# Kernel tuning notes

Measured on AMD Instinct MI355X. Metric: run time of the kernel, lower is better.

Reference implementation:

```python
import jax, jax.numpy as jnp
import numpy as np

N_NODES = 100000
N_EDGES = 1600000
IN_CH = 128
OUT_CH = 64
HID = 2 * OUT_CH  # 128


def setup_inputs() -> dict:
    key = jax.random.key(0)
    ks = jax.random.split(key, 8)
    s = lambda fan_in: 1.0 / np.sqrt(fan_in)
    return {
        "x": jax.random.normal(ks[0], (N_NODES, IN_CH), jnp.float32),
        "edge_index": jax.random.randint(ks[1], (2, N_EDGES), 0, N_NODES, dtype=jnp.int32),
        "W1": jax.random.normal(ks[2], (IN_CH, HID), jnp.float32) * s(IN_CH),
        "b1": jnp.zeros((HID,), jnp.float32),
        "W2": jax.random.normal(ks[3], (HID, HID), jnp.float32) * s(HID),
        "b2": jnp.zeros((HID,), jnp.float32),
        "W3": jax.random.normal(ks[4], (HID, OUT_CH), jnp.float32) * s(HID),
        "b3": jnp.zeros((OUT_CH,), jnp.float32),
    }


def reference(x, edge_index, W1, b1, W2, b2, W3, b3):
    N = x.shape[0]
    # GCNConv (PyG semantics): add self-loops, symmetric deg^{-1/2} normalization,
    # linear transform, scatter-add aggregation at destination, then bias.
    loops = jnp.arange(N, dtype=edge_index.dtype)
    src = jnp.concatenate([edge_index[0], loops])  # [E+N]
    dst = jnp.concatenate([edge_index[1], loops])  # [E+N]
    deg = jnp.zeros((N,), x.dtype).at[dst].add(1.0)  # in-degree incl. self-loop
    dinv = jnp.where(deg > 0, jax.lax.rsqrt(deg), 0.0)
    norm = (dinv[src] * dinv[dst])[:, None]  # [E+N, 1]

    def gcn_conv(h, W, b):
        h = h @ W  # transform first (smaller when out < in)
        msg = h[src] * norm  # gather + normalize, [E+N, C]
        agg = jnp.zeros((N, h.shape[1]), h.dtype).at[dst].add(msg)  # scatter-add
        return agg + b

    h = jax.nn.relu(gcn_conv(x, W1, b1))
    h = jax.nn.relu(gcn_conv(h, W2, b2))
    h = gcn_conv(h, W3, b3)
    return jnp.min(h, axis=0)  # min-pool over nodes -> [OUT_CH]
```

## Files before the change

### kernel.cpp

```cpp
#include <hip/hip_runtime.h>
#include <stdint.h>
#include <stddef.h>
#include <float.h>

typedef short bf16x8 __attribute__((ext_vector_type(8)));
typedef float f32x4 __attribute__((ext_vector_type(4)));

static __device__ __forceinline__ unsigned enc_min(float v) {
  unsigned u = __float_as_uint(v);
  return (u & 0x80000000u) ? ~u : (u | 0x80000000u);
}
static __device__ __forceinline__ unsigned short f2bf(float f) {
  unsigned u = __float_as_uint(f);
  u += 0x7fffu + ((u >> 16) & 1u);
  return (unsigned short)(u >> 16);
}
static __device__ __forceinline__ float bf2f(unsigned short b) {
  return __uint_as_float(((unsigned)b) << 16);
}
static __device__ __forceinline__ void acc8(float* a, uint4 v) {
  a[0] += __uint_as_float(v.x << 16);
  a[1] += __uint_as_float(v.x & 0xffff0000u);
  a[2] += __uint_as_float(v.y << 16);
  a[3] += __uint_as_float(v.y & 0xffff0000u);
  a[4] += __uint_as_float(v.z << 16);
  a[5] += __uint_as_float(v.z & 0xffff0000u);
  a[6] += __uint_as_float(v.w << 16);
  a[7] += __uint_as_float(v.w & 0xffff0000u);
}

__global__ __launch_bounds__(256) void k_count_bin(const int* __restrict__ edge, int E, int N,
                                                   int* __restrict__ cnt8,
                                                   int* __restrict__ bin_cur,
                                                   int2* __restrict__ pairs,
                                                   int binw, int bcap) {
  __shared__ int h[8], gbase[8], lfill[8];
  int cslot = blockIdx.x & 7;
  int* cnt = cnt8 + (size_t)cslot * N;
  int tid = threadIdx.x;
  int nt = (E + 1023) >> 10;
  for (int t = blockIdx.x; t < nt; t += gridDim.x) {
    int e0 = t << 10;
    if (tid < 8) { h[tid] = 0; lfill[tid] = 0; }
    __syncthreads();
    int d[4], s[4], g[4], r[4];
#pragma unroll
    for (int k = 0; k < 4; ++k) {
      int e = e0 + tid + k * 256;
      d[k] = -1;
      if (e < E) {
        d[k] = edge[E + e];
        s[k] = edge[e];
        g[k] = (int)((unsigned)d[k] / (unsigned)binw);
        r[k] = atomicAdd(&cnt[d[k]], 1);
        atomicAdd(&h[g[k]], 1);
      }
    }
    __syncthreads();
    if (tid < 8) gbase[tid] = atomicAdd(&bin_cur[tid], h[tid]);
    __syncthreads();
#pragma unroll
    for (int k = 0; k < 4; ++k) {
      if (d[k] >= 0) {
        int rr = atomicAdd(&lfill[g[k]], 1);
        int p = gbase[g[k]] + rr;
        unsigned packed = (unsigned)d[k] | ((unsigned)cslot << 17) | ((unsigned)r[k] << 20);
        if (p < bcap) pairs[(size_t)g[k] * bcap + p] = make_int2((int)packed, s[k]);
      }
    }
    __syncthreads();
  }
}

__global__ void k_scan1(const int* __restrict__ cnt8, int N,
                        int* __restrict__ cnt, int* __restrict__ incl,
                        int* __restrict__ bsum) {
  __shared__ int sm[1024];
  int tid = threadIdx.x;
  int i = blockIdx.x * 1024 + tid;
  int v = 0;
  if (i < N) {
#pragma unroll
    for (int g = 0; g < 8; ++g) v += cnt8[(size_t)g * N + i];
    cnt[i] = v;
  }
  sm[tid] = v;
  __syncthreads();
  for (int off = 1; off < 1024; off <<= 1) {
    int t = (tid >= off) ? sm[tid - off] : 0;
    __syncthreads();
    sm[tid] += t;
    __syncthreads();
  }
  if (i < N) incl[i] = sm[tid];
  if (tid == 1023) bsum[blockIdx.x] = sm[1023];
}

__global__ void k_scan2(const int* __restrict__ bsum, int nb, int* __restrict__ boff) {
  __shared__ int sm[128];
  int tid = threadIdx.x;
  int v = (tid < nb) ? bsum[tid] : 0;
  sm[tid] = v;
  __syncthreads();
  for (int off = 1; off < 128; off <<= 1) {
    int t = (tid >= off) ? sm[tid - off] : 0;
    __syncthreads();
    sm[tid] += t;
    __syncthreads();
  }
  if (tid < nb) boff[tid] = sm[tid] - v;
}

__global__ void k_aux(const int* __restrict__ cnt, const int* __restrict__ cnt8,
                      const int* __restrict__ incl, const int* __restrict__ boff,
                      int N, int E, int* __restrict__ row_ptr,
                      int* __restrict__ base8, float* __restrict__ dinv) {
  int i = blockIdx.x * blockDim.x + threadIdx.x;
  if (i < N) {
    int rp = incl[i] - cnt[i] + boff[i >> 10];
    row_ptr[i] = rp;
    dinv[i] = 1.0f / sqrtf((float)(cnt[i] + 1));
    int run = rp;
#pragma unroll
    for (int c = 0; c < 8; ++c) {
      base8[(size_t)c * N + i] = run;
      run += cnt8[(size_t)c * N + i];
    }
  } else if (i == N) {
    row_ptr[N] = E;
  }
}

__global__ void k_prepw(const float* __restrict__ W1, const float* __restrict__ W2,
                        const float* __restrict__ W3,
                        unsigned short* __restrict__ w1h, unsigned short* __restrict__ w1l,
                        unsigned short* __restrict__ w2h, unsigned short* __restrict__ w2l,
                        unsigned short* __restrict__ w3h, unsigned short* __restrict__ w3l) {
  const int K = 128;
  int idx = blockIdx.x * 256 + threadIdx.x;
  const float* W;
  unsigned short *oh, *ol;
  int Nn, base;
  if (idx < 16384) { W = W1; Nn = 128; oh = w1h; ol = w1l; base = idx; }
  else if (idx < 32768) { W = W2; Nn = 128; oh = w2h; ol = w2l; base = idx - 16384; }
  else if (idx < 40960) { W = W3; Nn = 64; oh = w3h; ol = w3l; base = idx - 32768; }
  else return;
  int n = base / K, k = base % K;
  float w = W[(size_t)k * Nn + n];
  unsigned short h = f2bf(w);
  unsigned short l = f2bf(w - bf2f(h));
  int nf = n >> 4, mloc = n & 15, kci = k >> 5, quad = (k >> 3) & 3, j = k & 7;
  size_t o = ((size_t)((nf * 4 + kci) * 64 + quad * 16 + mloc)) * 8 + j;
  oh[o] = h;
  ol[o] = l;
}

template <int NFW>
static __device__ __forceinline__ void gemm_body(const float* __restrict__ A,
                                                 const unsigned short* __restrict__ Wfh,
                                                 const unsigned short* __restrict__ Wfl,
                                                 const float* __restrict__ dinv,
                                                 unsigned short* __restrict__ P, int M,
                                                 int blk) {
  const int K = 128;
  const int COUT = NFW * 64;
  __shared__ unsigned short Ah[64][136];
  __shared__ unsigned short Al[64][136];
  int tid = threadIdx.x;
  int m0 = blk * 64;
  int w = tid >> 6, lane = tid & 63;

  bf16x8 bh[NFW][4], bl[NFW][4];
#pragma unroll
  for (int i = 0; i < NFW; ++i)
#pragma unroll
    for (int kci = 0; kci < 4; ++kci) {
      size_t o = ((size_t)(((w * NFW + i) * 4 + kci) * 64 + lane)) * 8;
      bh[i][kci] = *(const bf16x8*)&Wfh[o];
      bl[i][kci] = *(const bf16x8*)&Wfl[o];
    }

#pragma unroll
  for (int q = 0; q < 8; ++q) {
    int f = q * 256 + tid;
    int m = f >> 5, k4 = f & 31;
    int row = m0 + m;
    if (row >= M) row = M - 1;
    float4 v = *(const float4*)&A[(size_t)row * K + k4 * 4];
    unsigned short h0 = f2bf(v.x), h1 = f2bf(v.y), h2 = f2bf(v.z), h3 = f2bf(v.w);
    unsigned short l0 = f2bf(v.x - bf2f(h0)), l1 = f2bf(v.y - bf2f(h1));
    unsigned short l2 = f2bf(v.z - bf2f(h2)), l3 = f2bf(v.w - bf2f(h3));
    uint2 hh, ll;
    hh.x = (unsigned)h0 | ((unsigned)h1 << 16);
    hh.y = (unsigned)h2 | ((unsigned)h3 << 16);
    ll.x = (unsigned)l0 | ((unsigned)l1 << 16);
    ll.y = (unsigned)l2 | ((unsigned)l3 << 16);
    *(uint2*)&Ah[m][k4 * 4] = hh;
    *(uint2*)&Al[m][k4 * 4] = ll;
  }
  __syncthreads();

  int mloc = lane & 15, quad = lane >> 4;
  f32x4 acc[4][NFW];
#pragma unroll
  for (int rt = 0; rt < 4; ++rt)
#pragma unroll
    for (int i = 0; i < NFW; ++i) acc[rt][i] = (f32x4){0.f, 0.f, 0.f, 0.f};

#pragma unroll
  for (int rt = 0; rt < 4; ++rt) {
    const unsigned short* ph = &Ah[rt * 16 + mloc][quad * 8];
    const unsigned short* pl = &Al[rt * 16 + mloc][quad * 8];
#pragma unroll
    for (int kci = 0; kci < 4; ++kci) {
      bf16x8 ah = *(const bf16x8*)(ph + kci * 32);
      bf16x8 al = *(const bf16x8*)(pl + kci * 32);
#pragma unroll
      for (int i = 0; i < NFW; ++i) {
        acc[rt][i] = __builtin_amdgcn_mfma_f32_16x16x32_bf16(al, bh[i][kci], acc[rt][i], 0, 0, 0);
        acc[rt][i] = __builtin_amdgcn_mfma_f32_16x16x32_bf16(ah, bl[i][kci], acc[rt][i], 0, 0, 0);
        acc[rt][i] = __builtin_amdgcn_mfma_f32_16x16x32_bf16(ah, bh[i][kci], acc[rt][i], 0, 0, 0);
      }
    }
  }

#pragma unroll
  for (int rt = 0; rt < 4; ++rt) {
    int rbase = m0 + rt * 16 + quad * 4;
#pragma unroll
    for (int r = 0; r < 4; ++r) {
      int row = rbase + r;
      if (row < M) {
        float dv = dinv[row];
#pragma unroll
        for (int i = 0; i < NFW; ++i) {
          int nf = w * NFW + i;
          P[(size_t)row * COUT + nf * 16 + mloc] = f2bf(acc[rt][i][r] * dv);
        }
      }
    }
  }
}

__global__ __launch_bounds__(256) void k_fill_gemm(const float* __restrict__ A,
                                                   const unsigned short* __restrict__ Wfh,
                                                   const unsigned short* __restrict__ Wfl,
                                                   const float* __restrict__ dinv,
                                                   unsigned short* __restrict__ P, int M,
                                                   const int2* __restrict__ pairs,
                                                   const int* __restrict__ bin_cur, int bcap,
                                                   const int* __restrict__ base8, int N,
                                                   int* __restrict__ srcs, int ns) {
  if ((int)blockIdx.x >= ns) {
    gemm_body<2>(A, Wfh, Wfl, dinv, P, M, blockIdx.x - ns);
  } else {
    int grp = blockIdx.x & 7;
    int bslot = blockIdx.x >> 3;
    int nslot = ns >> 3;
    int cnt_g = bin_cur[grp];
    if (cnt_g > bcap) cnt_g = bcap;
    const int2* pp = pairs + (size_t)grp * bcap;
    for (int i = bslot * blockDim.x + threadIdx.x; i < cnt_g; i += nslot * blockDim.x) {
      int2 pr = pp[i];
      unsigned w = (unsigned)pr.x;
      int d = (int)(w & 0x1FFFFu);
      int c = (int)((w >> 17) & 7u);
      int r = (int)(w >> 20);
      srcs[base8[(size_t)c * N + d] + r] = pr.y;
    }
  }
}

template <int NFW>
__global__ __launch_bounds__(256) void k_agg_gemm(const unsigned short* __restrict__ Pin,
                                                  const int* __restrict__ row_ptr,
                                                  const int* __restrict__ srcs,
                                                  const float* __restrict__ dinv,
                                                  const float* __restrict__ bias,
                                                  const unsigned short* __restrict__ Wfh,
                                                  const unsigned short* __restrict__ Wfl,
                                                  unsigned short* __restrict__ Pout, int N) {
  const int COUT = NFW * 64;
  __shared__ unsigned short Ah[16][136];
  __shared__ unsigned short Al[16][136];
  int tid = threadIdx.x;
  int wv = tid >> 6, lane = tid & 63;
  int grp = lane >> 4, sub = lane & 15;
  int m = wv * 4 + grp;
  int d = blockIdx.x * 16 + m;
  int dc = d < N ? d : N - 1;
  bool valid = d < N;
  unsigned soff = (unsigned)sub * 16u;
  const char* Pb = (const char*)Pin;

  float a[8] = {0.f, 0.f, 0.f, 0.f, 0.f, 0.f, 0.f, 0.f};
  {
    uint4 v = *(const uint4*)(Pb + ((unsigned)dc * 256u + soff));
    acc8(a, v);
  }
  int lo = row_ptr[dc];
  int hi = row_ptr[valid ? d + 1 : dc];
  int j = lo;
  for (; j + 8 <= hi; j += 8) {
    unsigned id[8];
    uint4 vv[8];
#pragma unroll
    for (int k = 0; k < 8; ++k) id[k] = (unsigned)srcs[j + k];
#pragma unroll
    for (int k = 0; k < 8; ++k) vv[k] = *(const uint4*)(Pb + (id[k] * 256u + soff));
#pragma unroll
    for (int k = 0; k < 8; ++k) acc8(a, vv[k]);
  }
  for (; j + 4 <= hi; j += 4) {
    unsigned id[4];
    uint4 vv[4];
#pragma unroll
    for (int k = 0; k < 4; ++k) id[k] = (unsigned)srcs[j + k];
#pragma unroll
    for (int k = 0; k < 4; ++k) vv[k] = *(const uint4*)(Pb + (id[k] * 256u + soff));
#pragma unroll
    for (int k = 0; k < 4; ++k) acc8(a, vv[k]);
  }
  for (; j < hi; ++j) {
    unsigned i0 = (unsigned)srcs[j];
    uint4 v0 = *(const uint4*)(Pb + (i0 * 256u + soff));
    acc8(a, v0);
  }

  bf16x8 bh[NFW][4], bl[NFW][4];
#pragma unroll
  for (int i = 0; i < NFW; ++i)
#pragma unroll
    for (int kci = 0; kci < 4; ++kci) {
      size_t o = ((size_t)(((wv * NFW + i) * 4 + kci) * 64 + lane)) * 8;
      bh[i][kci] = *(const bf16x8*)&Wfh[o];
      bl[i][kci] = *(const bf16x8*)&Wfl[o];
    }

  float dv = dinv[dc];
  int ch0 = sub * 8;
  float4 bv0 = *(const float4*)&bias[ch0];
  float4 bv1 = *(const float4*)&bias[ch0 + 4];
  float h[8];
  h[0] = dv * a[0] + bv0.x; h[1] = dv * a[1] + bv0.y;
  h[2] = dv * a[2] + bv0.z; h[3] = dv * a[3] + bv0.w;
  h[4] = dv * a[4] + bv1.x; h[5] = dv * a[5] + bv1.y;
  h[6] = dv * a[6] + bv1.z; h[7] = dv * a[7] + bv1.w;
#pragma unroll
  for (int k = 0; k < 8; ++k) h[k] = fmaxf(h[k], 0.f);
  unsigned short hb[8], lb[8];
#pragma unroll
  for (int k = 0; k < 8; ++k) {
    hb[k] = f2bf(h[k]);
    lb[k] = f2bf(h[k] - bf2f(hb[k]));
  }
  uint4 HH, LL;
  HH.x = (unsigned)hb[0] | ((unsigned)hb[1] << 16);
  HH.y = (unsigned)hb[2] | ((unsigned)hb[3] << 16);
  HH.z = (unsigned)hb[4] | ((unsigned)hb[5] << 16);
  HH.w = (unsigned)hb[6] | ((unsigned)hb[7] << 16);
  LL.x = (unsigned)lb[0] | ((unsigned)lb[1] << 16);
  LL.y = (unsigned)lb[2] | ((unsigned)lb[3] << 16);
  LL.z = (unsigned)lb[4] | ((unsigned)lb[5] << 16);
  LL.w = (unsigned)lb[6] | ((unsigned)lb[7] << 16);
  *(uint4*)&Ah[m][ch0] = HH;
  *(uint4*)&Al[m][ch0] = LL;
  __syncthreads();

  int mloc = lane & 15, quad = lane >> 4;
  f32x4 acc[NFW];
#pragma unroll
  for (int i = 0; i < NFW; ++i) acc[i] = (f32x4){0.f, 0.f, 0.f, 0.f};
#pragma unroll
  for (int kci = 0; kci < 4; ++kci) {
    bf16x8 ah = *(const bf16x8*)&Ah[mloc][quad * 8 + kci * 32];
    bf16x8 al = *(const bf16x8*)&Al[mloc][quad * 8 + kci * 32];
#pragma unroll
    for (int i = 0; i < NFW; ++i) {
      acc[i] = __builtin_amdgcn_mfma_f32_16x16x32_bf16(al, bh[i][kci], acc[i], 0, 0, 0);
      acc[i] = __builtin_amdgcn_mfma_f32_16x16x32_bf16(ah, bl[i][kci], acc[i], 0, 0, 0);
      acc[i] = __builtin_amdgcn_mfma_f32_16x16x32_bf16(ah, bh[i][kci], acc[i], 0, 0, 0);
    }
  }
  int rbase = blockIdx.x * 16 + quad * 4;
#pragma unroll
  for (int r = 0; r < 4; ++r) {
    int row = rbase + r;
    if (row < N) {
      float dvr = dinv[row];
#pragma unroll
      for (int i = 0; i < NFW; ++i) {
        int nf = wv * NFW + i;
        Pout[(size_t)row * COUT + nf * 16 + mloc] = f2bf(acc[i][r] * dvr);
      }
    }
  }
}

__global__ __launch_bounds__(256) void k_agg_pool(const unsigned short* __restrict__ P,
                                                  const int* __restrict__ row_ptr,
                                                  const int* __restrict__ srcs,
                                                  const float* __restrict__ dinv,
                                                  const float* __restrict__ bias,
                                                  unsigned* __restrict__ minenc, int N) {
  const int CAP = 448;
  __shared__ int s_idx[4][CAP];
  __shared__ float s_red[4][32];
  int tid = threadIdx.x;
  int wv = tid >> 6, lane = tid & 63;
  int b8 = blockIdx.x & 7;
  int slice = b8 >> 2, part = b8 & 3;
  int g0 = ((blockIdx.x >> 3) * 4 + part) * 64 + wv * 16;
  const char* Pb = (const char*)P + slice * 64;

  int i = lane >> 2, q = lane & 3;
  unsigned qoff = (unsigned)q * 16u;
  int d = g0 + i;
  int dc = d < N ? d : N - 1;
  bool valid = d < N;

  int e0 = row_ptr[g0 < N ? g0 : N];
  int e1 = row_ptr[(g0 + 16) < N ? (g0 + 16) : N];
  int lo_n = row_ptr[dc];
  int hi_n = row_ptr[valid ? d + 1 : dc];

  float a[8];
  {
    uint4 v = *(const uint4*)(Pb + ((unsigned)dc * 128u + qoff));
    a[0] = __uint_as_float(v.x << 16);
    a[1] = __uint_as_float(v.x & 0xffff0000u);
    a[2] = __uint_as_float(v.y << 16);
    a[3] = __uint_as_float(v.y & 0xffff0000u);
    a[4] = __uint_as_float(v.z << 16);
    a[5] = __uint_as_float(v.z & 0xffff0000u);
    a[6] = __uint_as_float(v.w << 16);
    a[7] = __uint_as_float(v.w & 0xffff0000u);
  }

  for (int w0 = e0; w0 < e1; w0 += CAP) {
    int wend = min(w0 + CAP, e1);
    int cnt = wend - w0;
    __builtin_amdgcn_wave_barrier();
    for (int t = lane; t < cnt; t += 64) s_idx[wv][t] = srcs[w0 + t];
    __builtin_amdgcn_wave_barrier();
    int j = max(lo_n, w0), hi = min(hi_n, wend);
    for (; j + 4 <= hi; j += 4) {
      unsigned i0 = (unsigned)s_idx[wv][j - w0];
      unsigned i1 = (unsigned)s_idx[wv][j - w0 + 1];
      unsigned i2 = (unsigned)s_idx[wv][j - w0 + 2];
      unsigned i3 = (unsigned)s_idx[wv][j - w0 + 3];
      uint4 v0 = *(const uint4*)(Pb + (i0 * 128u + qoff));
      uint4 v1 = *(const uint4*)(Pb + (i1 * 128u + qoff));
      uint4 v2 = *(const uint4*)(Pb + (i2 * 128u + qoff));
      uint4 v3 = *(const uint4*)(Pb + (i3 * 128u + qoff));
      acc8(a, v0);
      acc8(a, v1);
      acc8(a, v2);
      acc8(a, v3);
    }
    for (; j < hi; ++j) {
      unsigned i0 = (unsigned)s_idx[wv][j - w0];
      uint4 v0 = *(const uint4*)(Pb + (i0 * 128u + qoff));
      acc8(a, v0);
    }
  }

  int c0 = slice * 32 + q * 8;
  float dv = dinv[dc];
  float4 bv0 = *(const float4*)&bias[c0];
  float4 bv1 = *(const float4*)&bias[c0 + 4];
  float h[8];
  h[0] = dv * a[0] + bv0.x; h[1] = dv * a[1] + bv0.y;
  h[2] = dv * a[2] + bv0.z; h[3] = dv * a[3] + bv0.w;
  h[4] = dv * a[4] + bv1.x; h[5] = dv * a[5] + bv1.y;
  h[6] = dv * a[6] + bv1.z; h[7] = dv * a[7] + bv1.w;

  if (!valid) {
#pragma unroll
    for (int k = 0; k < 8; ++k) h[k] = FLT_MAX;
  }
#pragma unroll
  for (int off = 4; off < 64; off <<= 1) {
#pragma unroll
    for (int k = 0; k < 8; ++k) h[k] = fminf(h[k], __shfl_xor(h[k], off, 64));
  }
  if (lane < 4) {
#pragma unroll
    for (int k = 0; k < 8; ++k) s_red[wv][q * 8 + k] = h[k];
  }
  __syncthreads();
  if (tid < 32) {
    float mn = fminf(fminf(s_red[0][tid], s_red[1][tid]),
                     fminf(s_red[2][tid], s_red[3][tid]));
    atomicMin(&minenc[slice * 32 + tid], enc_min(mn));
  }
}

__global__ void k_decode(const unsigned* __restrict__ minenc, float* __restrict__ out) {
  int c = threadIdx.x;
  unsigned k = minenc[c];
  unsigned u = (k & 0x80000000u) ? (k & 0x7FFFFFFFu) : ~k;
  out[c] = __uint_as_float(u);
}

extern "C" void kernel_launch(void* const* d_in, const int* in_sizes, int n_in,
                              void* d_out, int out_size, void* d_ws, size_t ws_size,
                              hipStream_t stream) {
  const float* X  = (const float*)d_in[0];
  const int* edge = (const int*)d_in[1];
  const float* W1 = (const float*)d_in[2];
  const float* b1 = (const float*)d_in[3];
  const float* W2 = (const float*)d_in[4];
  const float* b2 = (const float*)d_in[5];
  const float* W3 = (const float*)d_in[6];
  const float* b3 = (const float*)d_in[7];
  float* out = (float*)d_out;

  const int IN_CH = 128;
  int N = in_sizes[0] / IN_CH;
  int E = in_sizes[1] / 2;

  char* ws = (char*)d_ws;
  size_t off = 0;
  auto alloc = [&](size_t bytes) {
    void* p = ws + off;
    off = (off + bytes + 255) & ~(size_t)255;
    return p;
  };
  unsigned short* P1 = (unsigned short*)alloc((size_t)N * 128 * 2);
  unsigned short* P2 = (unsigned short*)alloc((size_t)N * 128 * 2);
  int* srcs      = (int*)alloc((size_t)E * 4);
  int* cnt8      = (int*)alloc((size_t)8 * N * 4);
  int* base8     = (int*)alloc((size_t)8 * N * 4);
  int* cnt       = (int*)alloc((size_t)N * 4);
  int* incl      = (int*)alloc((size_t)N * 4);
  int* row_ptr   = (int*)alloc((size_t)(N + 1) * 4);
  float* dinv    = (float*)alloc((size_t)N * 4);
  int* bsum      = (int*)alloc(1024);
  int* boff      = (int*)alloc(1024);
  int* bin_cur   = (int*)alloc(256);
  unsigned* minenc = (unsigned*)alloc(256);
  unsigned short* w1h = (unsigned short*)alloc(16384 * 2);
  unsigned short* w1l = (unsigned short*)alloc(16384 * 2);
  unsigned short* w2h = (unsigned short*)alloc(16384 * 2);
  unsigned short* w2l = (unsigned short*)alloc(16384 * 2);
  unsigned short* w3h = (unsigned short*)alloc(8192 * 2);
  unsigned short* w3l = (unsigned short*)alloc(8192 * 2);

  int bcap = E / 8 + 65536;
  int binw = (N + 7) / 8;
  int2* pairs = (int2*)P2;
  unsigned short* P3 = P1;

  hipMemsetAsync(cnt8, 0, (size_t)8 * N * 4, stream);
  hipMemsetAsync(bin_cur, 0, 32, stream);
  hipMemsetAsync(minenc, 0xFF, 64 * 4, stream);

  int nb = (N + 1023) / 1024;
  int gx = (N + 63) / 64;
  int ns = 1024;
  int gagg = (N + 15) / 16;
  int c64 = (N + 255) / 256;
  k_prepw<<<160, 256, 0, stream>>>(W1, W2, W3, w1h, w1l, w2h, w2l, w3h, w3l);
  k_count_bin<<<782, 256, 0, stream>>>(edge, E, N, cnt8, bin_cur, pairs, binw, bcap);
  k_scan1<<<nb, 1024, 0, stream>>>(cnt8, N, cnt, incl, bsum);
  k_scan2<<<1, 128, 0, stream>>>(bsum, nb, boff);
  k_aux<<<(N + 256) / 256, 256, 0, stream>>>(cnt, cnt8, incl, boff, N, E, row_ptr, base8, dinv);

  k_fill_gemm<<<ns + gx, 256, 0, stream>>>(X, w1h, w1l, dinv, P1, N,
                                           pairs, bin_cur, bcap, base8, N, srcs, ns);
  k_agg_gemm<2><<<gagg, 256, 0, stream>>>(P1, row_ptr, srcs, dinv, b1, w2h, w2l, P2, N);
  k_agg_gemm<1><<<gagg, 256, 0, stream>>>(P2, row_ptr, srcs, dinv, b2, w3h, w3l, P3, N);
  k_agg_pool<<<c64 * 8, 256, 0, stream>>>(P3, row_ptr, srcs, dinv, b3, minenc, N);
  k_decode<<<1, 64, 0, stream>>>(minenc, out);
}
```

Measured before the change: 420.6 us.

## Replace global-atomic CSR build with 256-bucket two-pass local sort

Rebuilds the destination-sorted CSR construction. Edges are first binned into 256 destination buckets using shared-memory histograms, then each bucket is counted, scanned and scattered within one block using shared-memory atomics. This removes the 8-way per-node global count arrays, the multi-kernel scan and the separate fill pass. The trade-off is that the first GEMM no longer overlaps with the fill, and correctness depends on binw fitting in 512 and bucket sizes staying under bcap.

```diff
diff --git a/kernel.cpp b/kernel.cpp
--- a/kernel.cpp
+++ b/kernel.cpp
@@ -5,6 +5,8 @@
 
 typedef short bf16x8 __attribute__((ext_vector_type(8)));
 typedef float f32x4 __attribute__((ext_vector_type(4)));
+
+#define NB 256
 
 static __device__ __forceinline__ unsigned enc_min(float v) {
   unsigned u = __float_as_uint(v);
@@ -29,105 +31,117 @@
   a[7] += __uint_as_float(v.w & 0xffff0000u);
 }
 
-__global__ __launch_bounds__(256) void k_count_bin(const int* __restrict__ edge, int E, int N,
-                                                   int* __restrict__ cnt8,
-                                                   int* __restrict__ bin_cur,
-                                                   int2* __restrict__ pairs,
-                                                   int binw, int bcap) {
-  __shared__ int h[8], gbase[8], lfill[8];
-  int cslot = blockIdx.x & 7;
-  int* cnt = cnt8 + (size_t)cslot * N;
+__global__ __launch_bounds__(256) void k_binA(const int* __restrict__ edge, int E,
+                                              int* __restrict__ bin_cur,
+                                              int2* __restrict__ pairs,
+                                              int binw, int bcap) {
+  __shared__ int h[NB], gbase[NB];
   int tid = threadIdx.x;
-  int nt = (E + 1023) >> 10;
-  for (int t = blockIdx.x; t < nt; t += gridDim.x) {
-    int e0 = t << 10;
-    if (tid < 8) { h[tid] = 0; lfill[tid] = 0; }
-    __syncthreads();
-    int d[4], s[4], g[4], r[4];
-#pragma unroll
-    for (int k = 0; k < 4; ++k) {
-      int e = e0 + tid + k * 256;
-      d[k] = -1;
-      if (e < E) {
-        d[k] = edge[E + e];
-        s[k] = edge[e];
-        g[k] = (int)((unsigned)d[k] / (unsigned)binw);
-        r[k] = atomicAdd(&cnt[d[k]], 1);
-        atomicAdd(&h[g[k]], 1);
-      }
-    }
-    __syncthreads();
-    if (tid < 8) gbase[tid] = atomicAdd(&bin_cur[tid], h[tid]);
-    __syncthreads();
-#pragma unroll
-    for (int k = 0; k < 4; ++k) {
-      if (d[k] >= 0) {
-        int rr = atomicAdd(&lfill[g[k]], 1);
-        int p = gbase[g[k]] + rr;
-        unsigned packed = (unsigned)d[k] | ((unsigned)cslot << 17) | ((unsigned)r[k] << 20);
-        if (p < bcap) pairs[(size_t)g[k] * bcap + p] = make_int2((int)packed, s[k]);
-      }
-    }
-    __syncthreads();
-  }
-}
-
-__global__ void k_scan1(const int* __restrict__ cnt8, int N,
-                        int* __restrict__ cnt, int* __restrict__ incl,
-                        int* __restrict__ bsum) {
-  __shared__ int sm[1024];
+  int base = blockIdx.x * 4096;
+  h[tid] = 0;
+  if (tid + 0 == tid) {}
+  __syncthreads();
+  int d_[16], s_[16], pk[16];
+#pragma unroll
+  for (int k = 0; k < 16; ++k) {
+    int e = base + k * 256 + tid;
+    d_[k] = -1;
+    if (e < E) {
+      int d = edge[E + e];
+      int s = edge[e];
+      int g = (int)((unsigned)d / (unsigned)binw);
+      int rk = atomicAdd(&h[g], 1);
+      pk[k] = (g << 16) | rk;
+      d_[k] = d;
+      s_[k] = s;
+    }
+  }
+  __syncthreads();
+  if (h[tid] > 0) gbase[tid] = atomicAdd(&bin_cur[tid * 16], h[tid]);
+  __syncthreads();
+#pragma unroll
+  for (int k = 0; k < 16; ++k) {
+    if (d_[k] >= 0) {
+      int g = pk[k] >> 16;
+      int rk = pk[k] & 0xffff;
+      int p = gbase[g] + rk;
+      if (p < bcap) pairs[(size_t)g * bcap + p] = make_int2(d_[k], s_[k]);
+    }
+  }
+}
+
+__global__ void k_scanB(const int* __restrict__ bin_cur, int* __restrict__ bucket_base) {
+  __shared__ int sm[NB];
   int tid = threadIdx.x;
-  int i = blockIdx.x * 1024 + tid;
-  int v = 0;
-  if (i < N) {
-#pragma unroll
-    for (int g = 0; g < 8; ++g) v += cnt8[(size_t)g * N + i];
-    cnt[i] = v;
-  }
+  int v = bin_cur[tid * 16];
   sm[tid] = v;
   __syncthreads();
-  for (int off = 1; off < 1024; off <<= 1) {
+  for (int off = 1; off < NB; off <<= 1) {
     int t = (tid >= off) ? sm[tid - off] : 0;
     __syncthreads();
     sm[tid] += t;
     __syncthreads();
   }
-  if (i < N) incl[i] = sm[tid];
-  if (tid == 1023) bsum[blockIdx.x] = sm[1023];
-}
-
-__global__ void k_scan2(const int* __restrict__ bsum, int nb, int* __restrict__ boff) {
-  __shared__ int sm[128];
+  bucket_base[tid] = sm[tid] - v;
+}
+
+__global__ __launch_bounds__(256) void k_buildB(const int2* __restrict__ pairs,
+                                                const int* __restrict__ bin_cur,
+                                                const int* __restrict__ bucket_base,
+                                                int bcap, int binw, int N, int E,
+                                                int* __restrict__ row_ptr,
+                                                float* __restrict__ dinv,
+                                                int* __restrict__ srcs) {
+  __shared__ int cnt_s[512], cur_s[512], sm[512];
   int tid = threadIdx.x;
-  int v = (tid < nb) ? bsum[tid] : 0;
-  sm[tid] = v;
-  __syncthreads();
-  for (int off = 1; off < 128; off <<= 1) {
-    int t = (tid >= off) ? sm[tid - off] : 0;
+  int b = blockIdx.x;
+  int d0 = b * binw;
+  int dcnt = N - d0;
+  if (dcnt > binw) dcnt = binw;
+  if (dcnt < 0) dcnt = 0;
+  int nb_e = bin_cur[b * 16];
+  if (nb_e > bcap) nb_e = bcap;
+  int bbase = bucket_base[b];
+  const int2* pp = pairs + (size_t)b * bcap;
+
+  cnt_s[tid] = 0;
+  cnt_s[tid + 256] = 0;
+  __syncthreads();
+  for (int i = tid; i < nb_e; i += 256) {
+    int2 pr = pp[i];
+    atomicAdd(&cnt_s[pr.x - d0], 1);
+  }
+  __syncthreads();
+  int c0 = cnt_s[tid], c1 = cnt_s[tid + 256];
+  sm[tid] = c0;
+  sm[tid + 256] = c1;
+  __syncthreads();
+  for (int off = 1; off < 512; off <<= 1) {
+    int t0 = (tid >= off) ? sm[tid - off] : 0;
+    int i1 = tid + 256;
+    int t1 = (i1 >= off) ? sm[i1 - off] : 0;
     __syncthreads();
-    sm[tid] += t;
+    sm[tid] += t0;
+    sm[i1] += t1;
     __syncthreads();
   }
-  if (tid < nb) boff[tid] = sm[tid] - v;
-}
-
-__global__ void k_aux(const int* __restrict__ cnt, const int* __restrict__ cnt8,
-                      const int* __restrict__ incl, const int* __restrict__ boff,
-                      int N, int E, int* __restrict__ row_ptr,
-                      int* __restrict__ base8, float* __restrict__ dinv) {
-  int i = blockIdx.x * blockDim.x + threadIdx.x;
-  if (i < N) {
-    int rp = incl[i] - cnt[i] + boff[i >> 10];
-    row_ptr[i] = rp;
-    dinv[i] = 1.0f / sqrtf((float)(cnt[i] + 1));
-    int run = rp;
-#pragma unroll
-    for (int c = 0; c < 8; ++c) {
-      base8[(size_t)c * N + i] = run;
-      run += cnt8[(size_t)c * N + i];
-    }
-  } else if (i == N) {
-    row_ptr[N] = E;
+  int e0 = sm[tid] - c0, e1 = sm[tid + 256] - c1;
+  if (tid < dcnt) {
+    row_ptr[d0 + tid] = bbase + e0;
+    dinv[d0 + tid] = 1.0f / sqrtf((float)(c0 + 1));
+  }
+  if (tid + 256 < dcnt) {
+    row_ptr[d0 + tid + 256] = bbase + e1;
+    dinv[d0 + tid + 256] = 1.0f / sqrtf((float)(c1 + 1));
+  }
+  cur_s[tid] = e0;
+  cur_s[tid + 256] = e1;
+  if (tid == 0 && d0 + dcnt == N) row_ptr[N] = E;
+  __syncthreads();
+  for (int i = tid; i < nb_e; i += 256) {
+    int2 pr = pp[i];
+    int slot = bbase + atomicAdd(&cur_s[pr.x - d0], 1);
+    srcs[slot] = pr.y;
   }
 }
 
@@ -242,33 +256,12 @@
   }
 }
 
-__global__ __launch_bounds__(256) void k_fill_gemm(const float* __restrict__ A,
-                                                   const unsigned short* __restrict__ Wfh,
-                                                   const unsigned short* __restrict__ Wfl,
-                                                   const float* __restrict__ dinv,
-                                                   unsigned short* __restrict__ P, int M,
-                                                   const int2* __restrict__ pairs,
-                                                   const int* __restrict__ bin_cur, int bcap,
-                                                   const int* __restrict__ base8, int N,
-                                                   int* __restrict__ srcs, int ns) {
-  if ((int)blockIdx.x >= ns) {
-    gemm_body<2>(A, Wfh, Wfl, dinv, P, M, blockIdx.x - ns);
-  } else {
-    int grp = blockIdx.x & 7;
-    int bslot = blockIdx.x >> 3;
-    int nslot = ns >> 3;
-    int cnt_g = bin_cur[grp];
-    if (cnt_g > bcap) cnt_g = bcap;
-    const int2* pp = pairs + (size_t)grp * bcap;
-    for (int i = bslot * blockDim.x + threadIdx.x; i < cnt_g; i += nslot * blockDim.x) {
-      int2 pr = pp[i];
-      unsigned w = (unsigned)pr.x;
-      int d = (int)(w & 0x1FFFFu);
-      int c = (int)((w >> 17) & 7u);
-      int r = (int)(w >> 20);
-      srcs[base8[(size_t)c * N + d] + r] = pr.y;
-    }
-  }
+__global__ __launch_bounds__(256) void k_gemm1(const float* __restrict__ A,
+                                               const unsigned short* __restrict__ Wfh,
+                                               const unsigned short* __restrict__ Wfl,
+                                               const float* __restrict__ dinv,
+                                               unsigned short* __restrict__ P, int M) {
+  gemm_body<2>(A, Wfh, Wfl, dinv, P, M, blockIdx.x);
 }
 
 template <int NFW>
@@ -530,15 +523,10 @@
   unsigned short* P1 = (unsigned short*)alloc((size_t)N * 128 * 2);
   unsigned short* P2 = (unsigned short*)alloc((size_t)N * 128 * 2);
   int* srcs      = (int*)alloc((size_t)E * 4);
-  int* cnt8      = (int*)alloc((size_t)8 * N * 4);
-  int* base8     = (int*)alloc((size_t)8 * N * 4);
-  int* cnt       = (int*)alloc((size_t)N * 4);
-  int* incl      = (int*)alloc((size_t)N * 4);
   int* row_ptr   = (int*)alloc((size_t)(N + 1) * 4);
   float* dinv    = (float*)alloc((size_t)N * 4);
-  int* bsum      = (int*)alloc(1024);
-  int* boff      = (int*)alloc(1024);
-  int* bin_cur   = (int*)alloc(256);
+  int* bin_cur   = (int*)alloc((size_t)NB * 16 * 4);
+  int* bucket_base = (int*)alloc((size_t)NB * 4);
   unsigned* minenc = (unsigned*)alloc(256);
   unsigned short* w1h = (unsigned short*)alloc(16384 * 2);
   unsigned short* w1l = (unsigned short*)alloc(16384 * 2);
@@ -547,28 +535,24 @@
   unsigned short* w3h = (unsigned short*)alloc(8192 * 2);
   unsigned short* w3l = (unsigned short*)alloc(8192 * 2);
 
-  int bcap = E / 8 + 65536;
-  int binw = (N + 7) / 8;
+  int binw = (N + NB - 1) / NB;
+  int bcap = E / NB + 1024;
   int2* pairs = (int2*)P2;
   unsigned short* P3 = P1;
 
-  hipMemsetAsync(cnt8, 0, (size_t)8 * N * 4, stream);
-  hipMemsetAsync(bin_cur, 0, 32, stream);
+  hipMemsetAsync(bin_cur, 0, (size_t)NB * 16 * 4, stream);
   hipMemsetAsync(minenc, 0xFF, 64 * 4, stream);
 
-  int nb = (N + 1023) / 1024;
   int gx = (N + 63) / 64;
-  int ns = 1024;
+  int nta = (E + 4095) / 4096;
   int gagg = (N + 15) / 16;
   int c64 = (N + 255) / 256;
   k_prepw<<<160, 256, 0, stream>>>(W1, W2, W3, w1h, w1l, w2h, w2l, w3h, w3l);
-  k_count_bin<<<782, 256, 0, stream>>>(edge, E, N, cnt8, bin_cur, pairs, binw, bcap);
-  k_scan1<<<nb, 1024, 0, stream>>>(cnt8, N, cnt, incl, bsum);
-  k_scan2<<<1, 128, 0, stream>>>(bsum, nb, boff);
-  k_aux<<<(N + 256) / 256, 256, 0, stream>>>(cnt, cnt8, incl, boff, N, E, row_ptr, base8, dinv);
-
-  k_fill_gemm<<<ns + gx, 256, 0, stream>>>(X, w1h, w1l, dinv, P1, N,
-                                           pairs, bin_cur, bcap, base8, N, srcs, ns);
+  k_binA<<<nta, 256, 0, stream>>>(edge, E, bin_cur, pairs, binw, bcap);
+  k_scanB<<<1, NB, 0, stream>>>(bin_cur, bucket_base);
+  k_buildB<<<NB, 256, 0, stream>>>(pairs, bin_cur, bucket_base, bcap, binw, N, E,
+                                   row_ptr, dinv, srcs);
+  k_gemm1<<<gx, 256, 0, stream>>>(X, w1h, w1l, dinv, P1, N);
   k_agg_gemm<2><<<gagg, 256, 0, stream>>>(P1, row_ptr, srcs, dinv, b1, w2h, w2l, P2, N);
   k_agg_gemm<1><<<gagg, 256, 0, stream>>>(P2, row_ptr, srcs, dinv, b2, w3h, w3l, P3, N);
   k_agg_pool<<<c64 * 8, 256, 0, stream>>>(P3, row_ptr, srcs, dinv, b3, minenc, N);
```

New measurement: 362.7 us. -13.8%, faster.
